# Optimization experiments

Measured on AMD Instinct MI355X. Metric: run time of the kernel, lower is better.

Reference implementation:

```python
import jax, jax.numpy as jnp
import numpy as np

B, T, D = 4, 2048, 1024
H, HD = 16, 64          # heads, head_dim
F = 2 * HD              # hedgehog feature dim
C = 64                  # chunk size (fla fused_chunk)
EPS = 1e-5


def setup_inputs() -> dict:
    key = jax.random.key(0)
    ks = jax.random.split(key, 8)
    s = 0.02
    return {
        "hidden_states": jax.random.normal(ks[0], (B, T, D), jnp.float32),
        "residual": jax.random.normal(ks[1], (B, T, D), jnp.float32),
        "norm_weight": jnp.ones((D,), jnp.float32),
        "w_q": jax.random.normal(ks[2], (D, D), jnp.float32) * s,
        "w_k": jax.random.normal(ks[3], (D, D), jnp.float32) * s,
        "w_v": jax.random.normal(ks[4], (D, D), jnp.float32) * s,
        "w_o": jax.random.normal(ks[5], (D, D), jnp.float32) * s,
        "hh_q_w": jnp.eye(HD, dtype=jnp.float32) + 0.01 * jax.random.normal(ks[6], (HD, HD), jnp.float32),
        "hh_q_b": jnp.zeros((HD,), jnp.float32),
        "hh_k_w": jnp.eye(HD, dtype=jnp.float32) + 0.01 * jax.random.normal(ks[7], (HD, HD), jnp.float32),
        "hh_k_b": jnp.zeros((HD,), jnp.float32),
    }


def _rmsnorm(x, w):
    var = jnp.mean(jnp.square(x), axis=-1, keepdims=True)
    return x * jax.lax.rsqrt(var + EPS) * w


def _hedgehog(x, w, b):
    # x: [B,H,T,HD]; learned linear then softmax over cat([y, -y])
    y = jnp.einsum('bhtd,ed->bhte', x, w) + b
    return jax.nn.softmax(jnp.concatenate([y, -y], axis=-1), axis=-1)  # [B,H,T,2*HD]


def reference(hidden_states, residual, norm_weight, w_q, w_k, w_v, w_o,
              hh_q_w, hh_q_b, hh_k_w, hh_k_b):
    # fused add + RMSNorm, prenorm, residual kept in fp32
    resid = (hidden_states + residual).astype(jnp.float32)
    x = _rmsnorm(resid, norm_weight).astype(hidden_states.dtype)

    def proj(w):  # [B,T,D] @ [D,D] -> [B,H,T,HD]
        return (x @ w).reshape(B, T, H, HD).transpose(0, 2, 1, 3)

    q = _hedgehog(proj(w_q), hh_q_w, hh_q_b)            # [B,H,T,F]
    k = _hedgehog(proj(w_k), hh_k_w, hh_k_b)            # [B,H,T,F]
    v = proj(w_v)                                        # [B,H,T,HD]
    q = q * (F ** -0.5)

    # chunked causal linear attention: o_t = phi(q_t) . sum_{s<=t} phi(k_s) v_s^T
    N = T // C
    qc = q.reshape(B, H, N, C, F)
    kc = k.reshape(B, H, N, C, F)
    vc = v.reshape(B, H, N, C, HD)

    kv = jnp.einsum('bhncf,bhncd->bhnfd', kc, vc)        # per-chunk state update
    S = jnp.cumsum(kv, axis=2)
    S_excl = jnp.concatenate([jnp.zeros_like(S[:, :, :1]), S[:, :, :-1]], axis=2)
    inter = jnp.einsum('bhncf,bhnfd->bhncd', qc, S_excl)

    scores = jnp.einsum('bhncf,bhnmf->bhncm', qc, kc)    # intra-chunk [C,C]
    tri = jnp.tril(jnp.ones((C, C), dtype=bool))
    scores = jnp.where(tri, scores, 0.0)
    intra = jnp.einsum('bhncm,bhnmd->bhncd', scores, vc)

    o = (inter + intra).reshape(B, H, T, HD).transpose(0, 2, 1, 3).reshape(B, T, D)
    o = o @ w_o
    return o, resid
```

## Files before the change

### kernel.cpp

```cpp
#include <hip/hip_runtime.h>
#include <math.h>

#define B_   4
#define T_   2048
#define D_   1024
#define H_   16
#define HD_  64
#define F_   128
#define C_   64
#define NCH  32
#define BT_  8192
#define BTD_ 8388608

typedef __bf16 bf16_t;
typedef __bf16 bf16x4 __attribute__((ext_vector_type(4)));
typedef __bf16 bf16x8 __attribute__((ext_vector_type(8)));
typedef float  f32x4  __attribute__((ext_vector_type(4)));

#define GLD16(gp, lp)                                                      \
  __builtin_amdgcn_global_load_lds(                                       \
      (const __attribute__((address_space(1))) unsigned int*)(const void*)(gp), \
      (__attribute__((address_space(3))) unsigned int*)(void*)(lp), 16, 0, 0)

__global__ __launch_bounds__(256) void k_transpose_all(
    const float* __restrict__ w_q, const float* __restrict__ w_k,
    const float* __restrict__ w_v, const float* __restrict__ w_o,
    const float* __restrict__ hhqw, const float* __restrict__ hhkw,
    bf16_t* __restrict__ wqkvT, bf16_t* __restrict__ woT,
    bf16_t* __restrict__ hhbf) {
  const int z = blockIdx.z;
  const int tid = threadIdx.x;
  if (z == 4) {
    const int gid = blockIdx.y * 16 + blockIdx.x;
    if (gid < 32) {
      const int i = gid * 256 + tid;
      const float v = (i < 4096) ? hhqw[i] : hhkw[i - 4096];
      hhbf[i] = (__bf16)v;
    }
    return;
  }
  const float* w = (z == 0) ? w_q : (z == 1) ? w_k : (z == 2) ? w_v : w_o;
  bf16_t* wT = (z < 3) ? (wqkvT + (size_t)z * D_ * D_) : woT;
  __shared__ float tile[64][65];
  const int n0 = blockIdx.x * 64;
  const int k0 = blockIdx.y * 64;
#pragma unroll
  for (int g = 0; g < 4; ++g) {
    const int k = g * 16 + (tid >> 4);
    float4 v = *(const float4*)(w + (size_t)(k0 + k) * D_ + n0 + (tid & 15) * 4);
    tile[k][(tid & 15) * 4 + 0] = v.x;
    tile[k][(tid & 15) * 4 + 1] = v.y;
    tile[k][(tid & 15) * 4 + 2] = v.z;
    tile[k][(tid & 15) * 4 + 3] = v.w;
  }
  __syncthreads();
#pragma unroll
  for (int g = 0; g < 4; ++g) {
    const int n = g * 16 + (tid >> 4);
    bf16x4 o;
#pragma unroll
    for (int i = 0; i < 4; ++i) o[i] = (__bf16)tile[(tid & 15) * 4 + i][n];
    *(bf16x4*)(wT + (size_t)(n0 + n) * D_ + k0 + (tid & 15) * 4) = o;
  }
}

__global__ __launch_bounds__(256) void k_add_rmsnorm(
    const float* __restrict__ hs, const float* __restrict__ res,
    const float* __restrict__ w, float* __restrict__ resid_out,
    bf16_t* __restrict__ x_out) {
  const int row = blockIdx.x;
  const size_t base = (size_t)row * D_;
  const int tid = threadIdx.x;
  float4 h4 = *(const float4*)(hs + base + tid * 4);
  float4 r4 = *(const float4*)(res + base + tid * 4);
  float4 s4;
  s4.x = h4.x + r4.x; s4.y = h4.y + r4.y;
  s4.z = h4.z + r4.z; s4.w = h4.w + r4.w;
  *(float4*)(resid_out + base + tid * 4) = s4;
  float ss = s4.x * s4.x + s4.y * s4.y + s4.z * s4.z + s4.w * s4.w;
#pragma unroll
  for (int off = 32; off > 0; off >>= 1) ss += __shfl_down(ss, off);
  __shared__ float red[4];
  if ((tid & 63) == 0) red[tid >> 6] = ss;
  __syncthreads();
  const float tot = red[0] + red[1] + red[2] + red[3];
  const float rstd = rsqrtf(tot * (1.0f / D_) + 1e-5f);
  float4 w4 = *(const float4*)(w + tid * 4);
  bf16x4 xo;
  xo[0] = (__bf16)(s4.x * rstd * w4.x);
  xo[1] = (__bf16)(s4.y * rstd * w4.y);
  xo[2] = (__bf16)(s4.z * rstd * w4.z);
  xo[3] = (__bf16)(s4.w * rstd * w4.w);
  *(bf16x4*)(x_out + base + tid * 4) = xo;
}

template <int F32OUT>
__global__ __launch_bounds__(256) void k_gemm_mfma(
    const bf16_t* __restrict__ A, const bf16_t* __restrict__ BTb,
    void* __restrict__ Cb) {
  __shared__ bf16_t As[2][128 * 32];
  __shared__ bf16_t Bs[2][128 * 32];
  const int z = blockIdx.z;
  const bf16_t* BT = BTb + (size_t)z * (D_ * D_);
  const int tid = threadIdx.x;
  const int lane = tid & 63;
  const int wave = tid >> 6;
  const int bm = (blockIdx.x * 8 + (blockIdx.y & 7)) * 128;
  const int bn = (blockIdx.y >> 3) * 128;
  const int wm = (wave >> 1) * 64;
  const int wn = (wave & 1) * 64;
  const int r0 = wave * 32 + (lane >> 2);
  const int ssw = (((lane >> 2) & 3) ^ (lane >> 4));
  const int scol = (((lane & 3) ^ ssw) << 3);
  const bf16_t* ap0 = A + (size_t)(bm + r0) * D_ + scol;
  const bf16_t* ap1 = A + (size_t)(bm + r0 + 16) * D_ + scol;
  const bf16_t* bp0 = BT + (size_t)(bn + r0) * D_ + scol;
  const bf16_t* bp1 = BT + (size_t)(bn + r0 + 16) * D_ + scol;
  const int lb0 = wave * 1024;
  const int lb1 = wave * 1024 + 512;
  const int frow = lane & 15;
  const int lhi = lane >> 4;
  const int rsw = ((frow & 3) ^ ((frow >> 2) & 3));
  const int rcol = ((lhi ^ rsw) << 3);

  f32x4 acc[4][4] = {};
  GLD16(ap0, &As[0][lb0]);
  GLD16(ap1, &As[0][lb1]);
  GLD16(bp0, &Bs[0][lb0]);
  GLD16(bp1, &Bs[0][lb1]);
  __syncthreads();

  for (int k0 = 0; k0 < D_; k0 += 32) {
    const int cur = (k0 >> 5) & 1;
    if (k0 + 32 < D_) {
      const int nxt = cur ^ 1;
      GLD16(ap0 + k0 + 32, &As[nxt][lb0]);
      GLD16(ap1 + k0 + 32, &As[nxt][lb1]);
      GLD16(bp0 + k0 + 32, &Bs[nxt][lb0]);
      GLD16(bp1 + k0 + 32, &Bs[nxt][lb1]);
    }
    bf16x8 af[4], bq[4];
#pragma unroll
    for (int i = 0; i < 4; ++i) {
      af[i] = *(const bf16x8*)(&As[cur][(wm + i * 16 + frow) * 32 + rcol]);
      bq[i] = *(const bf16x8*)(&Bs[cur][(wn + i * 16 + frow) * 32 + rcol]);
    }
#pragma unroll
    for (int i = 0; i < 4; ++i)
#pragma unroll
      for (int j = 0; j < 4; ++j)
        acc[i][j] = __builtin_amdgcn_mfma_f32_16x16x32_bf16(af[i], bq[j],
                                                            acc[i][j], 0, 0, 0);
    __syncthreads();
  }

  const int crow0 = bm + wm + (lane >> 4) * 4;
  const int ccol0 = bn + wn + (lane & 15);
#pragma unroll
  for (int i = 0; i < 4; ++i)
#pragma unroll
    for (int j = 0; j < 4; ++j) {
      const size_t rb = (size_t)(crow0 + i * 16) * D_ + ccol0 + j * 16;
#pragma unroll
      for (int r = 0; r < 4; ++r) {
        if (F32OUT)
          ((float*)Cb)[rb + (size_t)r * D_] = acc[i][j][r];
        else
          ((bf16_t*)Cb + (size_t)z * ((size_t)BT_ * D_))[rb + (size_t)r * D_] =
              (__bf16)acc[i][j][r];
      }
    }
}

__device__ __forceinline__ int swF(int f) { return (f & 7) ^ ((f >> 3) & 7); }

__global__ __launch_bounds__(256) void k_hedgehog_kv(
    const bf16_t* __restrict__ pq, const bf16_t* __restrict__ pk,
    const bf16_t* __restrict__ hhbf,
    const float* __restrict__ bq, const float* __restrict__ bk,
    const bf16_t* __restrict__ pv,
    bf16_t* __restrict__ outq, bf16_t* __restrict__ outk,
    bf16_t* __restrict__ kvout) {
  __shared__ bf16_t featT[128 * 64];
  __shared__ bf16_t vt[64 * 64];
  const int z = blockIdx.y;
  const bf16_t* p = z ? pk : pq;
  const bf16_t* wb = hhbf + z * 4096;
  const float* bias = z ? bk : bq;
  bf16_t* out = z ? outk : outq;
  const float scale = z ? 1.0f : 0.08838834764831845f;

  const int blk = blockIdx.x;
  const int n = blk % NCH;
  const int h = (blk / NCH) % H_;
  const int b = blk / (NCH * H_);
  const int tid = threadIdx.x;
  const int lane = tid & 63;
  const int wv = tid >> 6;
  const int l15 = lane & 15;
  const int lhi = lane >> 4;

  if (z) {
#pragma unroll
    for (int g = 0; g < 2; ++g) {
      int i8 = g * 256 + tid;
      int m = i8 >> 3, d8 = (i8 & 7) * 8;
      bf16x8 v8 = *(const bf16x8*)(pv + (size_t)(b * T_ + n * 64 + m) * D_ +
                                   h * 64 + d8);
#pragma unroll
      for (int jj = 0; jj < 8; ++jj) {
        int d = d8 + jj;
        vt[d * 64 + (m ^ ((d & 7) << 3))] = v8[jj];
      }
    }
  }

  const int trowA = n * 64 + wv * 16 + l15;
  bf16x8 pa[2];
#pragma unroll
  for (int s = 0; s < 2; ++s)
    pa[s] = *(const bf16x8*)(p + (size_t)(b * T_ + trowA) * D_ + h * 64 +
                             s * 32 + lhi * 8);
  f32x4 acc[4] = {};
#pragma unroll
  for (int j = 0; j < 4; ++j)
#pragma unroll
    for (int s = 0; s < 2; ++s) {
      bf16x8 wf = *(const bf16x8*)(wb + (16 * j + l15) * 64 + s * 32 + lhi * 8);
      acc[j] = __builtin_amdgcn_mfma_f32_16x16x32_bf16(pa[s], wf, acc[j], 0, 0, 0);
    }
  float be[4];
#pragma unroll
  for (int j = 0; j < 4; ++j) be[j] = bias[16 * j + l15];

#pragma unroll
  for (int r = 0; r < 4; ++r) {
    float y[4];
#pragma unroll
    for (int j = 0; j < 4; ++j) y[j] = acc[j][r] + be[j];
    float m = fmaxf(fmaxf(fabsf(y[0]), fabsf(y[1])),
                    fmaxf(fabsf(y[2]), fabsf(y[3])));
#pragma unroll
    for (int o = 1; o < 16; o <<= 1) m = fmaxf(m, __shfl_xor(m, o));
    float e1[4], e2[4], s = 0.f;
#pragma unroll
    for (int j = 0; j < 4; ++j) {
      e1[j] = __expf(y[j] - m);
      e2[j] = __expf(-y[j] - m);
      s += e1[j] + e2[j];
    }
#pragma unroll
    for (int o = 1; o < 16; o <<= 1) s += __shfl_xor(s, o);
    const float inv = scale / s;
    const int c = wv * 16 + lhi * 4 + r;
#pragma unroll
    for (int j = 0; j < 4; ++j) {
      const int f1 = 16 * j + l15, f2 = f1 + 64;
      featT[f1 * 64 + (((c >> 3) ^ swF(f1)) << 3) + (c & 7)] = (__bf16)(e1[j] * inv);
      featT[f2 * 64 + (((c >> 3) ^ swF(f2)) << 3) + (c & 7)] = (__bf16)(e2[j] * inv);
    }
  }
  __syncthreads();

  const size_t obase = (size_t)(b * H_ + h) * T_ + n * 64;
#pragma unroll
  for (int g = 0; g < 4; ++g) {
    int i8 = g * 256 + tid;
    int t = i8 >> 4, fc = i8 & 15;
    bf16x8 o8;
#pragma unroll
    for (int jj = 0; jj < 8; ++jj) {
      int f = fc * 8 + jj;
      o8[jj] = featT[f * 64 + (((t >> 3) ^ swF(f)) << 3) + (t & 7)];
    }
    *(bf16x8*)(out + (obase + t) * F_ + fc * 8) = o8;
  }

  if (z) {
    const int drow = wv * 16 + l15;
    f32x4 a2[8] = {};
#pragma unroll
    for (int s = 0; s < 2; ++s) {
      const int c0 = s * 32 + lhi * 8;
      bf16x8 va = *(const bf16x8*)(vt + drow * 64 + (c0 ^ ((drow & 7) << 3)));
#pragma unroll
      for (int j = 0; j < 8; ++j) {
        const int fr = j * 16 + l15;
        bf16x8 kb = *(const bf16x8*)(featT + fr * 64 +
                                     ((((c0 >> 3) ^ swF(fr))) << 3));
        a2[j] = __builtin_amdgcn_mfma_f32_16x16x32_bf16(va, kb, a2[j], 0, 0, 0);
      }
    }
    bf16_t* ob = kvout + (size_t)blk * 8192;
#pragma unroll
    for (int j = 0; j < 8; ++j)
#pragma unroll
      for (int r = 0; r < 4; ++r) {
        int d = wv * 16 + lhi * 4 + r, f = j * 16 + l15;
        ob[d * 128 + f] = (__bf16)a2[j][r];
      }
  }
}

__global__ __launch_bounds__(256) void k_cumsum_excl(bf16_t* __restrict__ kv) {
  const int bh = blockIdx.x >> 2;
  const int slice = blockIdx.x & 3;
  const int e = slice * 2048 + threadIdx.x * 8;
  bf16_t* base = kv + (size_t)bh * NCH * 8192 + e;
  bf16x8 vals[NCH];
#pragma unroll
  for (int n = 0; n < NCH; ++n) vals[n] = *(const bf16x8*)(base + (size_t)n * 8192);
  float run[8] = {};
#pragma unroll
  for (int n = 0; n < NCH; ++n) {
    bf16x8 o;
#pragma unroll
    for (int j = 0; j < 8; ++j) {
      o[j] = (__bf16)run[j];
      run[j] += (float)vals[n][j];
    }
    *(bf16x8*)(base + (size_t)n * 8192) = o;
  }
}

__global__ __launch_bounds__(256) void k_attn_chunk(
    const bf16_t* __restrict__ qf,
    const bf16_t* __restrict__ kf,
    const bf16_t* __restrict__ pv,
    const bf16_t* __restrict__ kvx,
    bf16_t* __restrict__ o_tmp) {
  __shared__ bf16_t kt[64 * 128];
  __shared__ bf16_t st[64 * 128];
  __shared__ bf16_t vt[64 * 64];
  __shared__ bf16_t scs[64 * 64];
  const int blk = blockIdx.x;
  const int n = blk % NCH;
  const int h = (blk / NCH) % H_;
  const int b = blk / (NCH * H_);
  const int tid = threadIdx.x;
  const int lane = tid & 63;
  const int wv = tid >> 6;
  const int l15 = lane & 15;
  const int lhi = lane >> 4;
  const size_t rowbase = (size_t)(b * H_ + h) * T_ + n * 64;
  const bf16_t* qb = qf + rowbase * F_;
  const bf16_t* kb = kf + rowbase * F_;
  const bf16_t* kvb = kvx + (size_t)blk * 8192;

#pragma unroll
  for (int g = 0; g < 4; ++g) {
    const int cl = g * 256 + tid;
    const int row = cl >> 4, pc = cl & 15;
    const int cc = pc ^ (row & 7);
    const int lb = (g * 256 + wv * 64) * 8;
    GLD16(kb + (size_t)row * F_ + cc * 8, kt + lb);
    GLD16(kvb + (size_t)row * F_ + cc * 8, st + lb);
  }
#pragma unroll
  for (int g = 0; g < 2; ++g) {
    int i8 = g * 256 + tid;
    int m = i8 >> 3, d8 = (i8 & 7) * 8;
    bf16x8 v8 = *(const bf16x8*)(pv + (size_t)(b * T_ + n * 64 + m) * D_ +
                                 h * 64 + d8);
#pragma unroll
    for (int jj = 0; jj < 8; ++jj) {
      int d = d8 + jj;
      vt[d * 64 + (m ^ ((d & 7) << 3))] = v8[jj];
    }
  }
  bf16x8 qa[4];
#pragma unroll
  for (int s = 0; s < 4; ++s)
    qa[s] = *(const bf16x8*)(qb + (wv * 16 + l15) * F_ + s * 32 + lhi * 8);

  __syncthreads();

  f32x4 accS[4] = {};
#pragma unroll
  for (int j = 0; j < 4; ++j) {
    const int tr = j * 16 + l15;
#pragma unroll
    for (int s = 0; s < 4; ++s) {
      bf16x8 kk = *(const bf16x8*)(kt + tr * 128 +
                                   (((s * 4 + lhi) ^ (tr & 7)) << 3));
      accS[j] = __builtin_amdgcn_mfma_f32_16x16x32_bf16(qa[s], kk, accS[j], 0, 0, 0);
    }
  }
#pragma unroll
  for (int j = 0; j < 4; ++j)
#pragma unroll
    for (int r = 0; r < 4; ++r) {
      int c = wv * 16 + lhi * 4 + r;
      int m = j * 16 + l15;
      float v = (m <= c) ? accS[j][r] : 0.f;
      scs[c * 64 + (m ^ ((c & 7) << 3))] = (__bf16)v;
    }

  f32x4 acc[4] = {};
#pragma unroll
  for (int j = 0; j < 4; ++j) {
    const int dr = j * 16 + l15;
#pragma unroll
    for (int s = 0; s < 4; ++s) {
      bf16x8 sv = *(const bf16x8*)(st + dr * 128 +
                                   (((s * 4 + lhi) ^ (dr & 7)) << 3));
      acc[j] = __builtin_amdgcn_mfma_f32_16x16x32_bf16(qa[s], sv, acc[j], 0, 0, 0);
    }
  }

  const int crow = wv * 16 + l15;
#pragma unroll
  for (int s2 = 0; s2 < 2; ++s2) {
    const int m0 = s2 * 32 + lhi * 8;
    bf16x8 sa = *(const bf16x8*)(scs + crow * 64 + (m0 ^ ((crow & 7) << 3)));
#pragma unroll
    for (int j = 0; j < 4; ++j) {
      const int dr = j * 16 + l15;
      bf16x8 vb = *(const bf16x8*)(vt + dr * 64 + (m0 ^ ((dr & 7) << 3)));
      acc[j] = __builtin_amdgcn_mfma_f32_16x16x32_bf16(sa, vb, acc[j], 0, 0, 0);
    }
  }

#pragma unroll
  for (int j = 0; j < 4; ++j)
#pragma unroll
    for (int r = 0; r < 4; ++r) {
      int c = wv * 16 + lhi * 4 + r, d = j * 16 + l15;
      o_tmp[(size_t)(b * T_ + n * 64 + c) * D_ + h * 64 + d] = (__bf16)acc[j][r];
    }
}

extern "C" void kernel_launch(void* const* d_in, const int* in_sizes, int n_in,
                              void* d_out, int out_size, void* d_ws, size_t ws_size,
                              hipStream_t stream) {
  const float* hs   = (const float*)d_in[0];
  const float* res  = (const float*)d_in[1];
  const float* nw   = (const float*)d_in[2];
  const float* w_q  = (const float*)d_in[3];
  const float* w_k  = (const float*)d_in[4];
  const float* w_v  = (const float*)d_in[5];
  const float* w_o  = (const float*)d_in[6];
  const float* hhqw = (const float*)d_in[7];
  const float* hhqb = (const float*)d_in[8];
  const float* hhkw = (const float*)d_in[9];
  const float* hhkb = (const float*)d_in[10];

  float* out       = (float*)d_out;
  float* o_final   = out;
  float* resid_out = out + BTD_;

  char* wsb = (char*)d_ws;
  bf16_t* x_bf  = (bf16_t*)(wsb);
  bf16_t* wqkvT = (bf16_t*)(wsb + (16ull << 20));
  bf16_t* woT   = (bf16_t*)(wsb + (22ull << 20));
  bf16_t* qf    = (bf16_t*)(wsb + (24ull << 20));
  bf16_t* kf    = (bf16_t*)(wsb + (56ull << 20));
  bf16_t* pqkv  = (bf16_t*)(wsb + (88ull << 20));
  bf16_t* pq    = pqkv;
  bf16_t* pk    = pqkv + (size_t)BTD_;
  bf16_t* pvb   = pqkv + (size_t)2 * BTD_;
  bf16_t* kv    = (bf16_t*)(wsb + (136ull << 20));
  bf16_t* hhbf  = (bf16_t*)(wsb + (168ull << 20));
  bf16_t* o_tmp = x_bf;

  k_transpose_all<<<dim3(16, 16, 5), 256, 0, stream>>>(
      w_q, w_k, w_v, w_o, hhqw, hhkw, wqkvT, woT, hhbf);

  k_add_rmsnorm<<<BT_, 256, 0, stream>>>(hs, res, nw, resid_out, x_bf);

  k_gemm_mfma<0><<<dim3(8, 64, 3), 256, 0, stream>>>(x_bf, wqkvT, (void*)pqkv);

  k_hedgehog_kv<<<dim3(2048, 2), 256, 0, stream>>>(pq, pk, hhbf, hhqb, hhkb,
                                                   pvb, qf, kf, kv);

  k_cumsum_excl<<<256, 256, 0, stream>>>(kv);

  k_attn_chunk<<<2048, 256, 0, stream>>>(qf, kf, pvb, kv, o_tmp);

  k_gemm_mfma<1><<<dim3(8, 64, 1), 256, 0, stream>>>(o_tmp, woT, (void*)o_final);
}
```

Baseline: 299.6 us.

## Recompute hedgehog features inside attention kernel instead of materializing q/k features

The hedgehog feature maps for q and k are no longer written to global memory. The kv-state kernel now computes only k features for its per-chunk state update. The attention chunk kernel recomputes both q and k features from the projections in LDS. This removes writing and re-reading two large bf16 feature tensors (B*H*T*128 each) and the q-half of the feature kernel grid. In exchange the k feature map is computed twice and the attention kernel's LDS footprint and register use grow.

```diff
diff --git a/kernel.cpp b/kernel.cpp
--- a/kernel.cpp
+++ b/kernel.cpp
@@ -21,6 +21,8 @@
   __builtin_amdgcn_global_load_lds(                                       \
       (const __attribute__((address_space(1))) unsigned int*)(const void*)(gp), \
       (__attribute__((address_space(3))) unsigned int*)(void*)(lp), 16, 0, 0)
+
+__device__ __forceinline__ int swF(int f) { return (f & 7) ^ ((f >> 3) & 7); }
 
 __global__ __launch_bounds__(256) void k_transpose_all(
     const float* __restrict__ w_q, const float* __restrict__ w_k,
@@ -172,24 +174,12 @@
     }
 }
 
-__device__ __forceinline__ int swF(int f) { return (f & 7) ^ ((f >> 3) & 7); }
-
-__global__ __launch_bounds__(256) void k_hedgehog_kv(
-    const bf16_t* __restrict__ pq, const bf16_t* __restrict__ pk,
-    const bf16_t* __restrict__ hhbf,
-    const float* __restrict__ bq, const float* __restrict__ bk,
-    const bf16_t* __restrict__ pv,
-    bf16_t* __restrict__ outq, bf16_t* __restrict__ outk,
+__global__ __launch_bounds__(256) void k_featkv(
+    const bf16_t* __restrict__ pk, const bf16_t* __restrict__ hhbf,
+    const float* __restrict__ bk, const bf16_t* __restrict__ pv,
     bf16_t* __restrict__ kvout) {
   __shared__ bf16_t featT[128 * 64];
   __shared__ bf16_t vt[64 * 64];
-  const int z = blockIdx.y;
-  const bf16_t* p = z ? pk : pq;
-  const bf16_t* wb = hhbf + z * 4096;
-  const float* bias = z ? bk : bq;
-  bf16_t* out = z ? outk : outq;
-  const float scale = z ? 1.0f : 0.08838834764831845f;
-
   const int blk = blockIdx.x;
   const int n = blk % NCH;
   const int h = (blk / NCH) % H_;
@@ -199,19 +189,18 @@
   const int wv = tid >> 6;
   const int l15 = lane & 15;
   const int lhi = lane >> 4;
-
-  if (z) {
-#pragma unroll
-    for (int g = 0; g < 2; ++g) {
-      int i8 = g * 256 + tid;
-      int m = i8 >> 3, d8 = (i8 & 7) * 8;
-      bf16x8 v8 = *(const bf16x8*)(pv + (size_t)(b * T_ + n * 64 + m) * D_ +
-                                   h * 64 + d8);
-#pragma unroll
-      for (int jj = 0; jj < 8; ++jj) {
-        int d = d8 + jj;
-        vt[d * 64 + (m ^ ((d & 7) << 3))] = v8[jj];
-      }
+  const bf16_t* wb = hhbf + 4096;
+
+#pragma unroll
+  for (int g = 0; g < 2; ++g) {
+    int i8 = g * 256 + tid;
+    int m = i8 >> 3, d8 = (i8 & 7) * 8;
+    bf16x8 v8 = *(const bf16x8*)(pv + (size_t)(b * T_ + n * 64 + m) * D_ +
+                                 h * 64 + d8);
+#pragma unroll
+    for (int jj = 0; jj < 8; ++jj) {
+      int d = d8 + jj;
+      vt[d * 64 + (m ^ ((d & 7) << 3))] = v8[jj];
     }
   }
 
@@ -219,7 +208,7 @@
   bf16x8 pa[2];
 #pragma unroll
   for (int s = 0; s < 2; ++s)
-    pa[s] = *(const bf16x8*)(p + (size_t)(b * T_ + trowA) * D_ + h * 64 +
+    pa[s] = *(const bf16x8*)(pk + (size_t)(b * T_ + trowA) * D_ + h * 64 +
                              s * 32 + lhi * 8);
   f32x4 acc[4] = {};
 #pragma unroll
@@ -231,7 +220,7 @@
     }
   float be[4];
 #pragma unroll
-  for (int j = 0; j < 4; ++j) be[j] = bias[16 * j + l15];
+  for (int j = 0; j < 4; ++j) be[j] = bk[16 * j + l15];
 
 #pragma unroll
   for (int r = 0; r < 4; ++r) {
@@ -251,7 +240,7 @@
     }
 #pragma unroll
     for (int o = 1; o < 16; o <<= 1) s += __shfl_xor(s, o);
-    const float inv = scale / s;
+    const float inv = 1.0f / s;
     const int c = wv * 16 + lhi * 4 + r;
 #pragma unroll
     for (int j = 0; j < 4; ++j) {
@@ -262,44 +251,28 @@
   }
   __syncthreads();
 
-  const size_t obase = (size_t)(b * H_ + h) * T_ + n * 64;
-#pragma unroll
-  for (int g = 0; g < 4; ++g) {
-    int i8 = g * 256 + tid;
-    int t = i8 >> 4, fc = i8 & 15;
-    bf16x8 o8;
-#pragma unroll
-    for (int jj = 0; jj < 8; ++jj) {
-      int f = fc * 8 + jj;
-      o8[jj] = featT[f * 64 + (((t >> 3) ^ swF(f)) << 3) + (t & 7)];
-    }
-    *(bf16x8*)(out + (obase + t) * F_ + fc * 8) = o8;
-  }
-
-  if (z) {
-    const int drow = wv * 16 + l15;
-    f32x4 a2[8] = {};
-#pragma unroll
-    for (int s = 0; s < 2; ++s) {
-      const int c0 = s * 32 + lhi * 8;
-      bf16x8 va = *(const bf16x8*)(vt + drow * 64 + (c0 ^ ((drow & 7) << 3)));
-#pragma unroll
-      for (int j = 0; j < 8; ++j) {
-        const int fr = j * 16 + l15;
-        bf16x8 kb = *(const bf16x8*)(featT + fr * 64 +
-                                     ((((c0 >> 3) ^ swF(fr))) << 3));
-        a2[j] = __builtin_amdgcn_mfma_f32_16x16x32_bf16(va, kb, a2[j], 0, 0, 0);
-      }
-    }
-    bf16_t* ob = kvout + (size_t)blk * 8192;
-#pragma unroll
-    for (int j = 0; j < 8; ++j)
-#pragma unroll
-      for (int r = 0; r < 4; ++r) {
-        int d = wv * 16 + lhi * 4 + r, f = j * 16 + l15;
-        ob[d * 128 + f] = (__bf16)a2[j][r];
-      }
-  }
+  const int drow = wv * 16 + l15;
+  f32x4 a2[8] = {};
+#pragma unroll
+  for (int s = 0; s < 2; ++s) {
+    const int c0 = s * 32 + lhi * 8;
+    bf16x8 va = *(const bf16x8*)(vt + drow * 64 + (c0 ^ ((drow & 7) << 3)));
+#pragma unroll
+    for (int j = 0; j < 8; ++j) {
+      const int fr = j * 16 + l15;
+      bf16x8 kb = *(const bf16x8*)(featT + fr * 64 +
+                                   ((((c0 >> 3) ^ swF(fr))) << 3));
+      a2[j] = __builtin_amdgcn_mfma_f32_16x16x32_bf16(va, kb, a2[j], 0, 0, 0);
+    }
+  }
+  bf16_t* ob = kvout + (size_t)blk * 8192;
+#pragma unroll
+  for (int j = 0; j < 8; ++j)
+#pragma unroll
+    for (int r = 0; r < 4; ++r) {
+      int d = wv * 16 + lhi * 4 + r, f = j * 16 + l15;
+      ob[d * 128 + f] = (__bf16)a2[j][r];
+    }
 }
 
 __global__ __launch_bounds__(256) void k_cumsum_excl(bf16_t* __restrict__ kv) {
@@ -324,12 +297,15 @@
 }
 
 __global__ __launch_bounds__(256) void k_attn_chunk(
-    const bf16_t* __restrict__ qf,
-    const bf16_t* __restrict__ kf,
+    const bf16_t* __restrict__ pq,
+    const bf16_t* __restrict__ pk,
     const bf16_t* __restrict__ pv,
+    const bf16_t* __restrict__ hhbf,
+    const float* __restrict__ bq, const float* __restrict__ bk,
     const bf16_t* __restrict__ kvx,
     bf16_t* __restrict__ o_tmp) {
-  __shared__ bf16_t kt[64 * 128];
+  __shared__ bf16_t featQ[64 * 128];
+  __shared__ bf16_t featK[64 * 128];
   __shared__ bf16_t st[64 * 128];
   __shared__ bf16_t vt[64 * 64];
   __shared__ bf16_t scs[64 * 64];
@@ -342,9 +318,6 @@
   const int wv = tid >> 6;
   const int l15 = lane & 15;
   const int lhi = lane >> 4;
-  const size_t rowbase = (size_t)(b * H_ + h) * T_ + n * 64;
-  const bf16_t* qb = qf + rowbase * F_;
-  const bf16_t* kb = kf + rowbase * F_;
   const bf16_t* kvb = kvx + (size_t)blk * 8192;
 
 #pragma unroll
@@ -353,7 +326,6 @@
     const int row = cl >> 4, pc = cl & 15;
     const int cc = pc ^ (row & 7);
     const int lb = (g * 256 + wv * 64) * 8;
-    GLD16(kb + (size_t)row * F_ + cc * 8, kt + lb);
     GLD16(kvb + (size_t)row * F_ + cc * 8, st + lb);
   }
 #pragma unroll
@@ -368,21 +340,79 @@
       vt[d * 64 + (m ^ ((d & 7) << 3))] = v8[jj];
     }
   }
+
+  const size_t prow = (size_t)(b * T_ + n * 64 + wv * 16 + l15) * D_ + h * 64;
+  bf16x8 paq[2], pak[2];
+#pragma unroll
+  for (int s = 0; s < 2; ++s) {
+    paq[s] = *(const bf16x8*)(pq + prow + s * 32 + lhi * 8);
+    pak[s] = *(const bf16x8*)(pk + prow + s * 32 + lhi * 8);
+  }
+  f32x4 aq[4] = {}, ak[4] = {};
+#pragma unroll
+  for (int j = 0; j < 4; ++j)
+#pragma unroll
+    for (int s = 0; s < 2; ++s) {
+      bf16x8 wqf = *(const bf16x8*)(hhbf + (16 * j + l15) * 64 + s * 32 + lhi * 8);
+      bf16x8 wkf = *(const bf16x8*)(hhbf + 4096 + (16 * j + l15) * 64 + s * 32 + lhi * 8);
+      aq[j] = __builtin_amdgcn_mfma_f32_16x16x32_bf16(paq[s], wqf, aq[j], 0, 0, 0);
+      ak[j] = __builtin_amdgcn_mfma_f32_16x16x32_bf16(pak[s], wkf, ak[j], 0, 0, 0);
+    }
+  float beq[4], bek[4];
+#pragma unroll
+  for (int j = 0; j < 4; ++j) {
+    beq[j] = bq[16 * j + l15];
+    bek[j] = bk[16 * j + l15];
+  }
+#pragma unroll
+  for (int r = 0; r < 4; ++r) {
+    const int c = wv * 16 + lhi * 4 + r;
+#pragma unroll
+    for (int qk = 0; qk < 2; ++qk) {
+      float y[4];
+#pragma unroll
+      for (int j = 0; j < 4; ++j)
+        y[j] = (qk ? ak[j][r] + bek[j] : aq[j][r] + beq[j]);
+      float m = fmaxf(fmaxf(fabsf(y[0]), fabsf(y[1])),
+                      fmaxf(fabsf(y[2]), fabsf(y[3])));
+#pragma unroll
+      for (int o = 1; o < 16; o <<= 1) m = fmaxf(m, __shfl_xor(m, o));
+      float e1[4], e2[4], s = 0.f;
+#pragma unroll
+      for (int j = 0; j < 4; ++j) {
+        e1[j] = __expf(y[j] - m);
+        e2[j] = __expf(-y[j] - m);
+        s += e1[j] + e2[j];
+      }
+#pragma unroll
+      for (int o = 1; o < 16; o <<= 1) s += __shfl_xor(s, o);
+      const float inv = (qk ? 1.0f : 0.08838834764831845f) / s;
+      bf16_t* ft = qk ? featK : featQ;
+#pragma unroll
+      for (int j = 0; j < 4; ++j) {
+        const int f1 = 16 * j + l15, f2 = f1 + 64;
+        ft[c * 128 + (((f1 >> 3) ^ swF(c)) << 3) + (f1 & 7)] = (__bf16)(e1[j] * inv);
+        ft[c * 128 + (((f2 >> 3) ^ swF(c)) << 3) + (f2 & 7)] = (__bf16)(e2[j] * inv);
+      }
+    }
+  }
+  __syncthreads();
+
+  const int crow = wv * 16 + l15;
   bf16x8 qa[4];
 #pragma unroll
   for (int s = 0; s < 4; ++s)
-    qa[s] = *(const bf16x8*)(qb + (wv * 16 + l15) * F_ + s * 32 + lhi * 8);
-
-  __syncthreads();
+    qa[s] = *(const bf16x8*)(featQ + crow * 128 +
+                             (((s * 4 + lhi) ^ swF(crow)) << 3));
 
   f32x4 accS[4] = {};
 #pragma unroll
   for (int j = 0; j < 4; ++j) {
-    const int tr = j * 16 + l15;
+    const int mr = j * 16 + l15;
 #pragma unroll
     for (int s = 0; s < 4; ++s) {
-      bf16x8 kk = *(const bf16x8*)(kt + tr * 128 +
-                                   (((s * 4 + lhi) ^ (tr & 7)) << 3));
+      bf16x8 kk = *(const bf16x8*)(featK + mr * 128 +
+                                   (((s * 4 + lhi) ^ swF(mr)) << 3));
       accS[j] = __builtin_amdgcn_mfma_f32_16x16x32_bf16(qa[s], kk, accS[j], 0, 0, 0);
     }
   }
@@ -408,7 +438,6 @@
     }
   }
 
-  const int crow = wv * 16 + l15;
 #pragma unroll
   for (int s2 = 0; s2 < 2; ++s2) {
     const int m0 = s2 * 32 + lhi * 8;
@@ -453,8 +482,6 @@
   bf16_t* x_bf  = (bf16_t*)(wsb);
   bf16_t* wqkvT = (bf16_t*)(wsb + (16ull << 20));
   bf16_t* woT   = (bf16_t*)(wsb + (22ull << 20));
-  bf16_t* qf    = (bf16_t*)(wsb + (24ull << 20));
-  bf16_t* kf    = (bf16_t*)(wsb + (56ull << 20));
   bf16_t* pqkv  = (bf16_t*)(wsb + (88ull << 20));
   bf16_t* pq    = pqkv;
   bf16_t* pk    = pqkv + (size_t)BTD_;
@@ -470,12 +497,12 @@
 
   k_gemm_mfma<0><<<dim3(8, 64, 3), 256, 0, stream>>>(x_bf, wqkvT, (void*)pqkv);
 
-  k_hedgehog_kv<<<dim3(2048, 2), 256, 0, stream>>>(pq, pk, hhbf, hhqb, hhkb,
-                                                   pvb, qf, kf, kv);
+  k_featkv<<<2048, 256, 0, stream>>>(pk, hhbf, hhkb, pvb, kv);
 
   k_cumsum_excl<<<256, 256, 0, stream>>>(kv);
 
-  k_attn_chunk<<<2048, 256, 0, stream>>>(qf, kf, pvb, kv, o_tmp);
+  k_attn_chunk<<<2048, 256, 0, stream>>>(pq, pk, pvb, hhbf, hhqb, hhkb,
+                                         kv, o_tmp);
 
   k_gemm_mfma<1><<<dim3(8, 64, 1), 256, 0, stream>>>(o_tmp, woT, (void*)o_final);
 }
```

Result: no change. 300.6 us (+0.3%).
